# Kernel optimization log

Hardware: AMD Instinct MI355X
Metric: run time of the kernel (lower is better)

The kernel has to match this reference:

```python
import jax, jax.numpy as jnp
import numpy as np

N_NODES = 50000
N_EDGES = 640000
D = 128
BN_EPS = 1e-5


def setup_inputs() -> dict:
    key = jax.random.key(0)
    ks = jax.random.split(key, 12)
    s = 0.05  # weight init scale
    inp = {
        "nh": jax.random.normal(ks[0], (N_NODES, D), jnp.float32),
        "eh": jax.random.normal(ks[1], (N_EDGES, D), jnp.float32),
        "edge_index": jax.random.randint(ks[2], (2, N_EDGES), 0, N_NODES, dtype=jnp.int32),
        # GIN eps parameters (init zeros, as nn.Parameter(torch.zeros(input_dim)))
        "nf_eps": jnp.zeros((D,), jnp.float32),
        "ef_eps": jnp.zeros((D,), jnp.float32),
        # node-feature MLP: Linear(D,D) -> relu -> Linear(D,D)
        "nf_W1": jax.random.normal(ks[3], (D, D), jnp.float32) * s,
        "nf_b1": jnp.zeros((D,), jnp.float32),
        "nf_W2": jax.random.normal(ks[4], (D, D), jnp.float32) * s,
        "nf_b2": jnp.zeros((D,), jnp.float32),
        # edge-feature MLP
        "ef_W1": jax.random.normal(ks[5], (D, D), jnp.float32) * s,
        "ef_b1": jnp.zeros((D,), jnp.float32),
        "ef_W2": jax.random.normal(ks[6], (D, D), jnp.float32) * s,
        "ef_b2": jnp.zeros((D,), jnp.float32),
        # BatchNorm1d affine params (training-mode batch stats)
        "nf_gamma": jnp.ones((D,), jnp.float32),
        "nf_beta": jnp.zeros((D,), jnp.float32),
        "ef_gamma": jnp.ones((D,), jnp.float32),
        "ef_beta": jnp.zeros((D,), jnp.float32),
    }
    return inp


def _mlp(x, W1, b1, W2, b2):
    return jnp.maximum(x @ W1 + b1, 0.0) @ W2 + b2


def _batchnorm(x, gamma, beta):
    # training-mode BatchNorm1d: biased batch variance
    mean = jnp.mean(x, axis=0)
    var = jnp.mean(jnp.square(x - mean), axis=0)
    return (x - mean) * jax.lax.rsqrt(var + BN_EPS) * gamma + beta


def reference(nh, eh, edge_index, nf_eps, ef_eps,
              nf_W1, nf_b1, nf_W2, nf_b2,
              ef_W1, ef_b1, ef_W2, ef_b2,
              nf_gamma, nf_beta, ef_gamma, ef_beta):
    src, dst = edge_index[0], edge_index[1]
    src_nh = nh[src]          # [E, D] gather
    dst_nh = nh[dst]          # [E, D] gather
    msg = src_nh + eh         # [E, D]
    attn = jnp.sum(msg * dst_nh, axis=-1)  # [E]

    # scatter_softmax over destination segments
    seg_max = jax.ops.segment_max(attn, dst, num_segments=N_NODES)  # [N]
    ex = jnp.exp(attn - seg_max[dst])
    seg_sum = jax.ops.segment_sum(ex, dst, num_segments=N_NODES)
    alpha = ex / seg_sum[dst]                                       # [E]

    # scatter_add of weighted source messages
    nz = jax.ops.segment_sum(src_nh * alpha[:, None], dst, num_segments=N_NODES)  # [N, D]

    n_h = (1.0 + nf_eps) * nh + nz
    e_h = (1.0 + ef_eps) * eh + nz[src] - nz[dst]

    n_h = _mlp(n_h, nf_W1, nf_b1, nf_W2, nf_b2)
    e_h = _mlp(e_h, ef_W1, ef_b1, ef_W2, ef_b2)

    n_h = _batchnorm(n_h, nf_gamma, nf_beta)
    e_h = _batchnorm(e_h, ef_gamma, ef_beta)
    return n_h, e_h
```

## Files before the change

### kernel.cpp

```cpp
#include <hip/hip_runtime.h>
#include <cstdint>
#include <cstddef>

#define ND      128
#define NNODES  50000
#define NEDGES  640000
#define BNEPS   1e-5f
#define CAP     64

typedef __attribute__((ext_vector_type(8))) short bf16x8;
typedef __attribute__((ext_vector_type(4))) short s16x4;
typedef __attribute__((ext_vector_type(4))) float f32x4;

__device__ __forceinline__ short f2bf(float x) {
    unsigned u = __float_as_uint(x);
    unsigned r = u + 0x7fffu + ((u >> 16) & 1u);
    return (short)(r >> 16);
}
__device__ __forceinline__ float bf2f(short h) {
    return __uint_as_float(((unsigned)(unsigned short)h) << 16);
}

__global__ __launch_bounds__(128) void prep_w_kernel(
    const float* __restrict__ W1, const float* __restrict__ W2,
    short* __restrict__ w1h, short* __restrict__ w1l,
    short* __restrict__ w2h, short* __restrict__ w2l) {
    int k = blockIdx.x;
    int n = threadIdx.x;
    const float* W = (k < 128) ? W1 : W2;
    int kk = k & 127;
    float v = W[(size_t)kk * ND + n];
    short h = f2bf(v);
    short l = f2bf(v - bf2f(h));
    short* ph = (k < 128) ? w1h : w2h;
    short* pl = (k < 128) ? w1l : w2l;
    ph[(size_t)n * ND + kk] = h;
    pl[(size_t)n * ND + kk] = l;
}

__global__ __launch_bounds__(256) void attn_kernel(
    const float* __restrict__ nh, const float* __restrict__ eh,
    const int* __restrict__ ei, float* __restrict__ attn) {
    int gid  = blockIdx.x * 256 + threadIdx.x;
    int e    = gid >> 6;
    int lane = threadIdx.x & 63;
    if (e >= NEDGES) return;
    int s = ei[e], d = ei[NEDGES + e];
    float2 sv = ((const float2*)(nh + (size_t)s * ND))[lane];
    float2 dv = ((const float2*)(nh + (size_t)d * ND))[lane];
    float2 ev = ((const float2*)(eh + (size_t)e * ND))[lane];
    float acc = (sv.x + ev.x) * dv.x + (sv.y + ev.y) * dv.y;
#pragma unroll
    for (int off = 32; off > 0; off >>= 1) acc += __shfl_down(acc, off, 64);
    if (lane == 0) attn[e] = acc;
}

__global__ __launch_bounds__(256) void csr_fill_kernel(
    const int* __restrict__ ei, int* __restrict__ deg, int* __restrict__ slots) {
    int e = blockIdx.x * 256 + threadIdx.x;
    if (e >= NEDGES) return;
    int d = ei[NEDGES + e];
    int pos = atomicAdd(&deg[d], 1);
    if (pos < CAP) slots[(size_t)d * CAP + pos] = e;
}

__global__ __launch_bounds__(256) void gather_nz_kernel(
    const float* __restrict__ nh, const int* __restrict__ ei,
    const float* __restrict__ attn, const int* __restrict__ deg,
    const int* __restrict__ slots, float* __restrict__ nz) {
    int node = blockIdx.x * 4 + (threadIdx.x >> 6);
    int lane = threadIdx.x & 63;
    if (node >= NNODES) return;
    int dg = deg[node];
    if (dg > CAP) dg = CAP;

    int   e  = -1, si = 0;
    float a  = -3.0e38f;
    if (lane < dg) {
        e  = slots[(size_t)node * CAP + lane];
        a  = attn[e];
        si = ei[e];
    }
    float m = a;
#pragma unroll
    for (int off = 32; off > 0; off >>= 1) m = fmaxf(m, __shfl_xor(m, off, 64));
    float ex = (lane < dg) ? __expf(a - m) : 0.f;
    float sum = ex;
#pragma unroll
    for (int off = 32; off > 0; off >>= 1) sum += __shfl_xor(sum, off, 64);
    float rs = (dg > 0) ? 1.f / sum : 0.f;

    float2 acc = make_float2(0.f, 0.f);
    for (int i = 0; i < dg; ++i) {
        float al = __shfl(ex, i, 64) * rs;
        int   sv = __shfl(si, i, 64);
        float2 x = ((const float2*)(nh + (size_t)sv * ND))[lane];
        acc.x += al * x.x;
        acc.y += al * x.y;
    }
    ((float2*)(nz + (size_t)node * ND))[lane] = acc;
}

#define LDA 136
template <int MODE>
__global__ __launch_bounds__(256) void fused_mlp(
    const float* __restrict__ X,
    const short* __restrict__ w1h, const short* __restrict__ w1l,
    const float* __restrict__ b1,
    const short* __restrict__ w2h, const short* __restrict__ w2l,
    const float* __restrict__ b2,
    float* __restrict__ out, int M,
    const float* __restrict__ eps, const float* __restrict__ nz,
    const int* __restrict__ ei,
    float* __restrict__ ssum, float* __restrict__ ssq) {
    __shared__ short Ah[64 * LDA];
    __shared__ short Al[64 * LDA];
    __shared__ float ls[ND], ls2[ND];
    __shared__ int   sIdx[2][64];

    int tid  = threadIdx.x;
    int lane = tid & 63;
    int wv   = tid >> 6;
    int cn   = lane & 15;
    int kg   = lane >> 4;
    int row0 = blockIdx.x * 64;
    int cbase = wv * 32;

    if (tid < ND) { ls[tid] = 0.f; ls2[tid] = 0.f; }
    if (MODE == 1 && tid < 64) {
        int r = row0 + tid;
        sIdx[0][tid] = ei[r];
        sIdx[1][tid] = ei[NEDGES + r];
    }
    __syncthreads();

    for (int i = tid; i < 64 * 32; i += 256) {
        int r   = i >> 5;
        int c   = (i & 31) << 2;
        int row = row0 + r;
        float4 v = make_float4(0.f, 0.f, 0.f, 0.f);
        if (row < M) {
            float4 xv = *(const float4*)(X + (size_t)row * ND + c);
            float4 e4 = *(const float4*)(eps + c);
            if (MODE == 0) {
                float4 zv = *(const float4*)(nz + (size_t)row * ND + c);
                v.x = (1.f + e4.x) * xv.x + zv.x;
                v.y = (1.f + e4.y) * xv.y + zv.y;
                v.z = (1.f + e4.z) * xv.z + zv.z;
                v.w = (1.f + e4.w) * xv.w + zv.w;
            } else {
                float4 zs = *(const float4*)(nz + (size_t)sIdx[0][r] * ND + c);
                float4 zd = *(const float4*)(nz + (size_t)sIdx[1][r] * ND + c);
                v.x = (1.f + e4.x) * xv.x + zs.x - zd.x;
                v.y = (1.f + e4.y) * xv.y + zs.y - zd.y;
                v.z = (1.f + e4.z) * xv.z + zs.z - zd.z;
                v.w = (1.f + e4.w) * xv.w + zs.w - zd.w;
            }
        }
        s16x4 hv, lv;
        hv.x = f2bf(v.x); lv.x = f2bf(v.x - bf2f(hv.x));
        hv.y = f2bf(v.y); lv.y = f2bf(v.y - bf2f(hv.y));
        hv.z = f2bf(v.z); lv.z = f2bf(v.z - bf2f(hv.z));
        hv.w = f2bf(v.w); lv.w = f2bf(v.w - bf2f(hv.w));
        *(s16x4*)&Ah[r * LDA + c] = hv;
        *(s16x4*)&Al[r * LDA + c] = lv;
    }

    bf16x8 bh[2][4], bl[2][4];
#pragma unroll
    for (int cb = 0; cb < 2; ++cb) {
        int n = cbase + cb * 16 + cn;
#pragma unroll
        for (int ks = 0; ks < 4; ++ks) {
            size_t o = (size_t)n * ND + ks * 32 + kg * 8;
            bh[cb][ks] = *(const bf16x8*)(w1h + o);
            bl[cb][ks] = *(const bf16x8*)(w1l + o);
        }
    }
    float b1c[2] = { b1[cbase + cn], b1[cbase + 16 + cn] };
    float b2c[2] = { b2[cbase + cn], b2[cbase + 16 + cn] };

    f32x4 acc[4][2];
#pragma unroll
    for (int rb = 0; rb < 4; ++rb)
#pragma unroll
        for (int cb = 0; cb < 2; ++cb) acc[rb][cb] = (f32x4){0.f, 0.f, 0.f, 0.f};

    __syncthreads();

#pragma unroll
    for (int ks = 0; ks < 4; ++ks) {
        bf16x8 ah[4], al[4];
#pragma unroll
        for (int rb = 0; rb < 4; ++rb) {
            int off = (rb * 16 + cn) * LDA + ks * 32 + kg * 8;
            ah[rb] = *(const bf16x8*)&Ah[off];
            al[rb] = *(const bf16x8*)&Al[off];
        }
#pragma unroll
        for (int rb = 0; rb < 4; ++rb)
#pragma unroll
            for (int cb = 0; cb < 2; ++cb) {
                acc[rb][cb] = __builtin_amdgcn_mfma_f32_16x16x32_bf16(ah[rb], bh[cb][ks], acc[rb][cb], 0, 0, 0);
                acc[rb][cb] = __builtin_amdgcn_mfma_f32_16x16x32_bf16(ah[rb], bl[cb][ks], acc[rb][cb], 0, 0, 0);
                acc[rb][cb] = __builtin_amdgcn_mfma_f32_16x16x32_bf16(al[rb], bh[cb][ks], acc[rb][cb], 0, 0, 0);
            }
    }

    __syncthreads();

#pragma unroll
    for (int cb = 0; cb < 2; ++cb) {
        int n = cbase + cb * 16 + cn;
#pragma unroll
        for (int ks = 0; ks < 4; ++ks) {
            size_t o = (size_t)n * ND + ks * 32 + kg * 8;
            bh[cb][ks] = *(const bf16x8*)(w2h + o);
            bl[cb][ks] = *(const bf16x8*)(w2l + o);
        }
    }

#pragma unroll
    for (int rb = 0; rb < 4; ++rb)
#pragma unroll
        for (int cb = 0; cb < 2; ++cb)
#pragma unroll
            for (int r = 0; r < 4; ++r) {
                float v = acc[rb][cb][r] + b1c[cb];
                v = fmaxf(v, 0.f);
                short h = f2bf(v);
                short l = f2bf(v - bf2f(h));
                int row = rb * 16 + kg * 4 + r;
                int col = cbase + cb * 16 + cn;
                Ah[row * LDA + col] = h;
                Al[row * LDA + col] = l;
                acc[rb][cb][r] = 0.f;
            }
    __syncthreads();

#pragma unroll
    for (int ks = 0; ks < 4; ++ks) {
        bf16x8 ah[4], al[4];
#pragma unroll
        for (int rb = 0; rb < 4; ++rb) {
            int off = (rb * 16 + cn) * LDA + ks * 32 + kg * 8;
            ah[rb] = *(const bf16x8*)&Ah[off];
            al[rb] = *(const bf16x8*)&Al[off];
        }
#pragma unroll
        for (int rb = 0; rb < 4; ++rb)
#pragma unroll
            for (int cb = 0; cb < 2; ++cb) {
                acc[rb][cb] = __builtin_amdgcn_mfma_f32_16x16x32_bf16(ah[rb], bh[cb][ks], acc[rb][cb], 0, 0, 0);
                acc[rb][cb] = __builtin_amdgcn_mfma_f32_16x16x32_bf16(ah[rb], bl[cb][ks], acc[rb][cb], 0, 0, 0);
                acc[rb][cb] = __builtin_amdgcn_mfma_f32_16x16x32_bf16(al[rb], bh[cb][ks], acc[rb][cb], 0, 0, 0);
            }
    }

#pragma unroll
    for (int cb = 0; cb < 2; ++cb) {
        int col = cbase + cb * 16 + cn;
        float s = 0.f, s2 = 0.f;
#pragma unroll
        for (int rb = 0; rb < 4; ++rb)
#pragma unroll
            for (int r = 0; r < 4; ++r) {
                float v = acc[rb][cb][r] + b2c[cb];
                int row = row0 + rb * 16 + kg * 4 + r;
                if (row < M) {
                    out[(size_t)row * ND + col] = v;
                    s += v; s2 += v * v;
                }
            }
        atomicAdd(&ls[col], s);
        atomicAdd(&ls2[col], s2);
    }
    __syncthreads();
    if (tid < ND) {
        unsafeAtomicAdd(&ssum[tid], ls[tid]);
        unsafeAtomicAdd(&ssq[tid], ls2[tid]);
    }
}

__global__ void bn_finalize_kernel(float* __restrict__ sum, float* __restrict__ sumsq,
                                   const float* __restrict__ g, const float* __restrict__ b,
                                   float M) {
    int c = threadIdx.x;
    float mean  = sum[c] / M;
    float var   = sumsq[c] / M - mean * mean;
    float scale = g[c] * rsqrtf(var + BNEPS);
    sum[c]   = scale;
    sumsq[c] = b[c] - mean * scale;
}

__global__ __launch_bounds__(256) void bn_apply_kernel(
    float* __restrict__ x, int M,
    const float* __restrict__ scale, const float* __restrict__ shift) {
    size_t total4 = (size_t)M * (ND / 4);
    for (size_t i = (size_t)blockIdx.x * 256 + threadIdx.x; i < total4;
         i += (size_t)gridDim.x * 256) {
        int c = ((int)(i & 31)) << 2;
        float4 v = ((const float4*)x)[i];
        v.x = v.x * scale[c]     + shift[c];
        v.y = v.y * scale[c + 1] + shift[c + 1];
        v.z = v.z * scale[c + 2] + shift[c + 2];
        v.w = v.w * scale[c + 3] + shift[c + 3];
        ((float4*)x)[i] = v;
    }
}

extern "C" void kernel_launch(void* const* d_in, const int* in_sizes, int n_in,
                              void* d_out, int out_size, void* d_ws, size_t ws_size,
                              hipStream_t stream) {
    const float* nh       = (const float*)d_in[0];
    const float* eh       = (const float*)d_in[1];
    const int*   ei       = (const int*)d_in[2];
    const float* nf_eps   = (const float*)d_in[3];
    const float* ef_eps   = (const float*)d_in[4];
    const float* nf_W1    = (const float*)d_in[5];
    const float* nf_b1    = (const float*)d_in[6];
    const float* nf_W2    = (const float*)d_in[7];
    const float* nf_b2    = (const float*)d_in[8];
    const float* ef_W1    = (const float*)d_in[9];
    const float* ef_b1    = (const float*)d_in[10];
    const float* ef_W2    = (const float*)d_in[11];
    const float* ef_b2    = (const float*)d_in[12];
    const float* nf_gamma = (const float*)d_in[13];
    const float* nf_beta  = (const float*)d_in[14];
    const float* ef_gamma = (const float*)d_in[15];
    const float* ef_beta  = (const float*)d_in[16];

    float* out_n = (float*)d_out;
    float* out_e = (float*)d_out + (size_t)NNODES * ND;

    char* ws = (char*)d_ws;
    size_t off = 0;
    auto alloc = [&](size_t bytes) -> void* {
        void* p = ws + off;
        off = (off + bytes + 255) & ~(size_t)255;
        return p;
    };
    float* attn   = (float*)alloc((size_t)NEDGES * 4);
    float* nz     = (float*)alloc((size_t)NNODES * ND * 4);
    int*   deg    = (int*)alloc((size_t)NNODES * 4);
    int*   slots  = (int*)alloc((size_t)NNODES * CAP * 4);
    float* ssum_n = (float*)alloc(ND * 4);
    float* ssq_n  = (float*)alloc(ND * 4);
    float* ssum_e = (float*)alloc(ND * 4);
    float* ssq_e  = (float*)alloc(ND * 4);
    short* nw1h   = (short*)alloc((size_t)ND * ND * 2);
    short* nw1l   = (short*)alloc((size_t)ND * ND * 2);
    short* nw2h   = (short*)alloc((size_t)ND * ND * 2);
    short* nw2l   = (short*)alloc((size_t)ND * ND * 2);
    short* ew1h   = (short*)alloc((size_t)ND * ND * 2);
    short* ew1l   = (short*)alloc((size_t)ND * ND * 2);
    short* ew2h   = (short*)alloc((size_t)ND * ND * 2);
    short* ew2l   = (short*)alloc((size_t)ND * ND * 2);

    hipMemsetAsync(deg,    0, (size_t)NNODES * 4, stream);
    hipMemsetAsync(ssum_n, 0, ND * 4, stream);
    hipMemsetAsync(ssq_n,  0, ND * 4, stream);
    hipMemsetAsync(ssum_e, 0, ND * 4, stream);
    hipMemsetAsync(ssq_e,  0, ND * 4, stream);

    prep_w_kernel<<<256, 128, 0, stream>>>(nf_W1, nf_W2, nw1h, nw1l, nw2h, nw2l);
    prep_w_kernel<<<256, 128, 0, stream>>>(ef_W1, ef_W2, ew1h, ew1l, ew2h, ew2l);

    attn_kernel<<<NEDGES / 4, 256, 0, stream>>>(nh, eh, ei, attn);
    csr_fill_kernel<<<(NEDGES + 255) / 256, 256, 0, stream>>>(ei, deg, slots);
    gather_nz_kernel<<<(NNODES + 3) / 4, 256, 0, stream>>>(nh, ei, attn, deg, slots, nz);

    fused_mlp<0><<<(NNODES + 63) / 64, 256, 0, stream>>>(
        nh, nw1h, nw1l, nf_b1, nw2h, nw2l, nf_b2, out_n, NNODES,
        nf_eps, nz, nullptr, ssum_n, ssq_n);
    fused_mlp<1><<<NEDGES / 64, 256, 0, stream>>>(
        eh, ew1h, ew1l, ef_b1, ew2h, ew2l, ef_b2, out_e, NEDGES,
        ef_eps, nz, ei, ssum_e, ssq_e);

    bn_finalize_kernel<<<1, 128, 0, stream>>>(ssum_n, ssq_n, nf_gamma, nf_beta, (float)NNODES);
    bn_finalize_kernel<<<1, 128, 0, stream>>>(ssum_e, ssq_e, ef_gamma, ef_beta, (float)NEDGES);
    bn_apply_kernel<<<2048, 256, 0, stream>>>(out_n, NNODES, ssum_n, ssq_n);
    bn_apply_kernel<<<8192, 256, 0, stream>>>(out_e, NEDGES, ssum_e, ssq_e);
}
```

Baseline: 1.277 ms.

## Swizzle MLP LDS tiles, widen attn loads, drop BN-cancelled bias, shuffle-reduce stats

The MLP kernel's padded LDS layout is replaced by an XOR swizzle on unpadded 128-column tiles, to avoid bank conflicts while using less shared memory. Edge indices are now read directly instead of being staged in shared memory, which removes a barrier. Block-level BN statistics now use wave shuffles feeding global atomics, removing the LDS atomics and the final barrier. The second-layer bias is dropped because training-mode BatchNorm subtracts the per-column mean and cancels it exactly. The attention kernel moves to float4 loads with 32 lanes per edge, giving fewer shuffle steps and wider memory transactions.

```diff
diff --git a/kernel.cpp b/kernel.cpp
--- a/kernel.cpp
+++ b/kernel.cpp
@@ -19,6 +19,9 @@
 }
 __device__ __forceinline__ float bf2f(short h) {
     return __uint_as_float(((unsigned)(unsigned short)h) << 16);
+}
+__device__ __forceinline__ int swz(int row, int colbyte) {
+    return colbyte ^ ((row & 7) << 4);
 }
 
 __global__ __launch_bounds__(128) void prep_w_kernel(
@@ -41,18 +44,19 @@
 __global__ __launch_bounds__(256) void attn_kernel(
     const float* __restrict__ nh, const float* __restrict__ eh,
     const int* __restrict__ ei, float* __restrict__ attn) {
-    int gid  = blockIdx.x * 256 + threadIdx.x;
-    int e    = gid >> 6;
-    int lane = threadIdx.x & 63;
+    int gid = blockIdx.x * 256 + threadIdx.x;
+    int e   = gid >> 5;
+    int l   = threadIdx.x & 31;
     if (e >= NEDGES) return;
     int s = ei[e], d = ei[NEDGES + e];
-    float2 sv = ((const float2*)(nh + (size_t)s * ND))[lane];
-    float2 dv = ((const float2*)(nh + (size_t)d * ND))[lane];
-    float2 ev = ((const float2*)(eh + (size_t)e * ND))[lane];
-    float acc = (sv.x + ev.x) * dv.x + (sv.y + ev.y) * dv.y;
-#pragma unroll
-    for (int off = 32; off > 0; off >>= 1) acc += __shfl_down(acc, off, 64);
-    if (lane == 0) attn[e] = acc;
+    float4 sv = ((const float4*)(nh + (size_t)s * ND))[l];
+    float4 dv = ((const float4*)(nh + (size_t)d * ND))[l];
+    float4 ev = ((const float4*)(eh + (size_t)e * ND))[l];
+    float acc = (sv.x + ev.x) * dv.x + (sv.y + ev.y) * dv.y +
+                (sv.z + ev.z) * dv.z + (sv.w + ev.w) * dv.w;
+#pragma unroll
+    for (int off = 16; off > 0; off >>= 1) acc += __shfl_down(acc, off, 32);
+    if (l == 0) attn[e] = acc;
 }
 
 __global__ __launch_bounds__(256) void csr_fill_kernel(
@@ -101,22 +105,18 @@
     ((float2*)(nz + (size_t)node * ND))[lane] = acc;
 }
 
-#define LDA 136
 template <int MODE>
 __global__ __launch_bounds__(256) void fused_mlp(
     const float* __restrict__ X,
     const short* __restrict__ w1h, const short* __restrict__ w1l,
     const float* __restrict__ b1,
     const short* __restrict__ w2h, const short* __restrict__ w2l,
-    const float* __restrict__ b2,
     float* __restrict__ out, int M,
     const float* __restrict__ eps, const float* __restrict__ nz,
     const int* __restrict__ ei,
     float* __restrict__ ssum, float* __restrict__ ssq) {
-    __shared__ short Ah[64 * LDA];
-    __shared__ short Al[64 * LDA];
-    __shared__ float ls[ND], ls2[ND];
-    __shared__ int   sIdx[2][64];
+    __shared__ short Ah[64 * 128];
+    __shared__ short Al[64 * 128];
 
     int tid  = threadIdx.x;
     int lane = tid & 63;
@@ -126,20 +126,14 @@
     int row0 = blockIdx.x * 64;
     int cbase = wv * 32;
 
-    if (tid < ND) { ls[tid] = 0.f; ls2[tid] = 0.f; }
-    if (MODE == 1 && tid < 64) {
-        int r = row0 + tid;
-        sIdx[0][tid] = ei[r];
-        sIdx[1][tid] = ei[NEDGES + r];
-    }
-    __syncthreads();
-
-    for (int i = tid; i < 64 * 32; i += 256) {
+#pragma unroll
+    for (int k = 0; k < 8; ++k) {
+        int i   = tid + k * 256;
         int r   = i >> 5;
         int c   = (i & 31) << 2;
         int row = row0 + r;
         float4 v = make_float4(0.f, 0.f, 0.f, 0.f);
-        if (row < M) {
+        if (MODE == 1 || row < M) {
             float4 xv = *(const float4*)(X + (size_t)row * ND + c);
             float4 e4 = *(const float4*)(eps + c);
             if (MODE == 0) {
@@ -149,8 +143,9 @@
                 v.z = (1.f + e4.z) * xv.z + zv.z;
                 v.w = (1.f + e4.w) * xv.w + zv.w;
             } else {
-                float4 zs = *(const float4*)(nz + (size_t)sIdx[0][r] * ND + c);
-                float4 zd = *(const float4*)(nz + (size_t)sIdx[1][r] * ND + c);
+                int s = ei[row], d = ei[NEDGES + row];
+                float4 zs = *(const float4*)(nz + (size_t)s * ND + c);
+                float4 zd = *(const float4*)(nz + (size_t)d * ND + c);
                 v.x = (1.f + e4.x) * xv.x + zs.x - zd.x;
                 v.y = (1.f + e4.y) * xv.y + zs.y - zd.y;
                 v.z = (1.f + e4.z) * xv.z + zs.z - zd.z;
@@ -162,8 +157,9 @@
         hv.y = f2bf(v.y); lv.y = f2bf(v.y - bf2f(hv.y));
         hv.z = f2bf(v.z); lv.z = f2bf(v.z - bf2f(hv.z));
         hv.w = f2bf(v.w); lv.w = f2bf(v.w - bf2f(hv.w));
-        *(s16x4*)&Ah[r * LDA + c] = hv;
-        *(s16x4*)&Al[r * LDA + c] = lv;
+        int boff = (r << 8) + swz(r, c << 1);
+        *(s16x4*)((char*)Ah + boff) = hv;
+        *(s16x4*)((char*)Al + boff) = lv;
     }
 
     bf16x8 bh[2][4], bl[2][4];
@@ -178,7 +174,6 @@
         }
     }
     float b1c[2] = { b1[cbase + cn], b1[cbase + 16 + cn] };
-    float b2c[2] = { b2[cbase + cn], b2[cbase + 16 + cn] };
 
     f32x4 acc[4][2];
 #pragma unroll
@@ -193,9 +188,10 @@
         bf16x8 ah[4], al[4];
 #pragma unroll
         for (int rb = 0; rb < 4; ++rb) {
-            int off = (rb * 16 + cn) * LDA + ks * 32 + kg * 8;
-            ah[rb] = *(const bf16x8*)&Ah[off];
-            al[rb] = *(const bf16x8*)&Al[off];
+            int arow = rb * 16 + cn;
+            int aoff = (arow << 8) + swz(arow, (ks << 6) + (kg << 4));
+            ah[rb] = *(const bf16x8*)((const char*)Ah + aoff);
+            al[rb] = *(const bf16x8*)((const char*)Al + aoff);
         }
 #pragma unroll
         for (int rb = 0; rb < 4; ++rb)
@@ -230,10 +226,11 @@
                 v = fmaxf(v, 0.f);
                 short h = f2bf(v);
                 short l = f2bf(v - bf2f(h));
-                int row = rb * 16 + kg * 4 + r;
-                int col = cbase + cb * 16 + cn;
-                Ah[row * LDA + col] = h;
-                Al[row * LDA + col] = l;
+                int hrow  = rb * 16 + kg * 4 + r;
+                int hcolb = (cbase + cb * 16 + cn) << 1;
+                int hoff  = (hrow << 8) + swz(hrow, hcolb);
+                *(short*)((char*)Ah + hoff) = h;
+                *(short*)((char*)Al + hoff) = l;
                 acc[rb][cb][r] = 0.f;
             }
     __syncthreads();
@@ -243,9 +240,10 @@
         bf16x8 ah[4], al[4];
 #pragma unroll
         for (int rb = 0; rb < 4; ++rb) {
-            int off = (rb * 16 + cn) * LDA + ks * 32 + kg * 8;
-            ah[rb] = *(const bf16x8*)&Ah[off];
-            al[rb] = *(const bf16x8*)&Al[off];
+            int arow = rb * 16 + cn;
+            int aoff = (arow << 8) + swz(arow, (ks << 6) + (kg << 4));
+            ah[rb] = *(const bf16x8*)((const char*)Ah + aoff);
+            al[rb] = *(const bf16x8*)((const char*)Al + aoff);
         }
 #pragma unroll
         for (int rb = 0; rb < 4; ++rb)
@@ -265,20 +263,21 @@
         for (int rb = 0; rb < 4; ++rb)
 #pragma unroll
             for (int r = 0; r < 4; ++r) {
-                float v = acc[rb][cb][r] + b2c[cb];
+                float v = acc[rb][cb][r];
                 int row = row0 + rb * 16 + kg * 4 + r;
                 if (row < M) {
                     out[(size_t)row * ND + col] = v;
                     s += v; s2 += v * v;
                 }
             }
-        atomicAdd(&ls[col], s);
-        atomicAdd(&ls2[col], s2);
-    }
-    __syncthreads();
-    if (tid < ND) {
-        unsafeAtomicAdd(&ssum[tid], ls[tid]);
-        unsafeAtomicAdd(&ssq[tid], ls2[tid]);
+        s  += __shfl_down(s, 32, 64);
+        s  += __shfl_down(s, 16, 64);
+        s2 += __shfl_down(s2, 32, 64);
+        s2 += __shfl_down(s2, 16, 64);
+        if (kg == 0) {
+            unsafeAtomicAdd(&ssum[col], s);
+            unsafeAtomicAdd(&ssq[col], s2);
+        }
     }
 }
 
@@ -366,15 +365,15 @@
     prep_w_kernel<<<256, 128, 0, stream>>>(nf_W1, nf_W2, nw1h, nw1l, nw2h, nw2l);
     prep_w_kernel<<<256, 128, 0, stream>>>(ef_W1, ef_W2, ew1h, ew1l, ew2h, ew2l);
 
-    attn_kernel<<<NEDGES / 4, 256, 0, stream>>>(nh, eh, ei, attn);
+    attn_kernel<<<NEDGES / 8, 256, 0, stream>>>(nh, eh, ei, attn);
     csr_fill_kernel<<<(NEDGES + 255) / 256, 256, 0, stream>>>(ei, deg, slots);
     gather_nz_kernel<<<(NNODES + 3) / 4, 256, 0, stream>>>(nh, ei, attn, deg, slots, nz);
 
     fused_mlp<0><<<(NNODES + 63) / 64, 256, 0, stream>>>(
-        nh, nw1h, nw1l, nf_b1, nw2h, nw2l, nf_b2, out_n, NNODES,
+        nh, nw1h, nw1l, nf_b1, nw2h, nw2l, out_n, NNODES,
         nf_eps, nz, nullptr, ssum_n, ssq_n);
     fused_mlp<1><<<NEDGES / 64, 256, 0, stream>>>(
-        eh, ew1h, ew1l, ef_b1, ew2h, ew2l, ef_b2, out_e, NEDGES,
+        eh, ew1h, ew1l, ef_b1, ew2h, ew2l, out_e, NEDGES,
         ef_eps, nz, ei, ssum_e, ssq_e);
 
     bn_finalize_kernel<<<1, 128, 0, stream>>>(ssum_n, ssq_n, nf_gamma, nf_beta, (float)NNODES);
```

After: 1.167 ms. 8.6% less time.
